# Performance work log

Hardware: AMD Instinct MI355X
Metric: run time of the kernel (lower is better)

## Reference

```python
import jax, jax.numpy as jnp
import numpy as np
from jax import lax

VOCAB = 1000
TMAX = 1001  # max_episode_length + 1
L = 2048
H_GRU = 256


def setup_inputs() -> dict:
    key = jax.random.key(0)
    ks = jax.random.split(key, 40)
    g = lambda i, shape, s: jax.random.normal(ks[i], shape, dtype=jnp.float32) * s
    inp = {
        "x": jax.random.normal(ks[0], (1, 3, 124, 124), dtype=jnp.float32),
        "curr_instr": jax.random.randint(ks[1], (1, L), 0, VOCAB),
        "prev_instr": jax.random.randint(ks[2], (1, L), 0, VOCAB),
        "next_instr": jax.random.randint(ks[3], (1, L), 0, VOCAB),
        "tx": jax.random.randint(ks[4], (1,), 0, TMAX),
        "hx": jnp.zeros((1, 768), jnp.float32),
        "cx": jnp.zeros((1, 768), jnp.float32),
        # conv stack
        "conv1_w": g(5, (128, 3, 8, 8), 0.05), "conv1_b": jnp.zeros((128,), jnp.float32),
        "conv2_w": g(6, (64, 128, 4, 4), 0.03), "conv2_b": jnp.zeros((64,), jnp.float32),
        "conv3_w": g(7, (64, 64, 4, 4), 0.03), "conv3_b": jnp.zeros((64,), jnp.float32),
        # embeddings
        "emb": g(8, (VOCAB, 32), 0.1),
        "time_emb": g(9, (TMAX, 32), 0.1),
        # GRU (torch nn.GRU layout: 3*H rows for r,z,n)
        "gru_w_ih": g(10, (3 * H_GRU, 32), 0.1), "gru_w_hh": g(11, (3 * H_GRU, H_GRU), 0.06),
        "gru_b_ih": jnp.zeros((3 * H_GRU,), jnp.float32), "gru_b_hh": jnp.zeros((3 * H_GRU,), jnp.float32),
        # attention linear 256 -> 64
        "attn_w": g(12, (64, H_GRU), 0.06), "attn_b": jnp.zeros((64,), jnp.float32),
        # image-fusion linear 64*6*6 -> 256
        "lin_w": g(13, (256, 64 * 6 * 6), 0.02), "lin_b": jnp.zeros((256,), jnp.float32),
        # LSTMCell 768 -> 768 (torch layout: 4*H rows for i,f,g,o)
        "lstm_w_ih": g(14, (4 * 768, 768), 0.03), "lstm_w_hh": g(15, (4 * 768, 768), 0.03),
        "lstm_b_ih": jnp.zeros((4 * 768,), jnp.float32), "lstm_b_hh": jnp.zeros((4 * 768,), jnp.float32),
        # heads over [hx, time_emb] = 768 + 32 = 800
        "critic_w": g(16, (1, 800), 0.03), "critic_b": jnp.zeros((1,), jnp.float32),
        "actor_w": g(17, (4, 800), 0.01), "actor_b": jnp.zeros((4,), jnp.float32),
    }
    return inp


def _conv(x, w, b, s):
    return lax.conv_general_dilated(x, w, (s, s), "VALID") + b[None, :, None, None]


def reference(x, curr_instr, prev_instr, next_instr, tx, hx, cx,
              conv1_w, conv1_b, conv2_w, conv2_b, conv3_w, conv3_b,
              emb, time_emb, gru_w_ih, gru_w_hh, gru_b_ih, gru_b_hh,
              attn_w, attn_b, lin_w, lin_b,
              lstm_w_ih, lstm_w_hh, lstm_b_ih, lstm_b_hh,
              critic_w, critic_b, actor_w, actor_b):
    # image tower: [1,3,124,124] -> [1,64,6,6]
    h1 = jax.nn.relu(_conv(x, conv1_w, conv1_b, 4))
    h2 = jax.nn.relu(_conv(h1, conv2_w, conv2_b, 2))
    x_image_rep = jax.nn.relu(_conv(h2, conv3_w, conv3_b, 2))

    # three instruction sequences, encoded by a shared GRU (vmapped scan)
    tokens = jnp.stack([curr_instr[0], prev_instr[0], next_instr[0]])  # [3, L]

    def gru_encode(tok):
        xs = emb[tok]                               # [L, 32]
        gi_all = xs @ gru_w_ih.T + gru_b_ih         # precompute input gates [L, 3H]
        def step(h, gi):
            gh = h @ gru_w_hh.T + gru_b_hh
            i_r, i_z, i_n = jnp.split(gi, 3)
            h_r, h_z, h_n = jnp.split(gh, 3)
            r = jax.nn.sigmoid(i_r + h_r)
            z = jax.nn.sigmoid(i_z + h_z)
            n = jnp.tanh(i_n + r * h_n)
            return (1.0 - z) * n + z * h, None
        h, _ = lax.scan(step, jnp.zeros((H_GRU,), xs.dtype), gi_all)
        return h

    h3 = jax.vmap(gru_encode)(tokens)               # [3, 256]
    attn = jax.nn.sigmoid(h3 @ attn_w.T + attn_b)   # [3, 64]

    # BUG-FAITHFUL: original forward uses cached_computation['curr_x_attention']
    # for all three branches, so the three fused features are identical.
    curr_attn = attn[0][None, :, None, None]        # [1,64,1,1]
    fused = (x_image_rep * curr_attn).reshape(1, -1)  # [1, 2304]
    feat = jax.nn.relu(fused @ lin_w.T + lin_b)     # [1, 256]
    xcat = jnp.concatenate([feat, feat, feat], axis=1)  # [1, 768]

    # LSTMCell
    gates = xcat @ lstm_w_ih.T + lstm_b_ih + hx @ lstm_w_hh.T + lstm_b_hh  # [1, 3072]
    gi, gf, gg, go = jnp.split(gates, 4, axis=1)
    cx_new = jax.nn.sigmoid(gf) * cx + jax.nn.sigmoid(gi) * jnp.tanh(gg)
    hx_new = jax.nn.sigmoid(go) * jnp.tanh(cx_new)

    t = time_emb[tx].reshape(-1, 32)                # [1, 32]
    z = jnp.concatenate([hx_new, t], axis=1)        # [1, 800]
    critic = z @ critic_w.T + critic_b              # [1, 1]
    actor = z @ actor_w.T + actor_b                 # [1, 4]
    return critic, actor, hx_new, cx_new
```

## Files before the change

### kernel.cpp

```cpp
#include <hip/hip_runtime.h>
#include <hip/hip_bf16.h>
#include <stdint.h>


typedef _Float16 half8 __attribute__((ext_vector_type(8)));
typedef _Float16 half2v __attribute__((ext_vector_type(2)));
typedef float f32x4 __attribute__((ext_vector_type(4)));

__device__ __forceinline__ float sigm(float x) { return 1.0f / (1.0f + __expf(-x)); }
__device__ __forceinline__ float tanh_f(float x) { return 2.0f / (1.0f + __expf(-2.0f * x)) - 1.0f; }

__global__ void k_pack(const float* __restrict__ whh, uint32_t* __restrict__ wf16p) {
    int i = blockIdx.x * 256 + threadIdx.x;
    if (i >= 98304) return;
    half2v p = {(_Float16)whh[2 * i], (_Float16)whh[2 * i + 1]};
    wf16p[i] = __builtin_bit_cast(uint32_t, p);
}

__global__ void k_conv1(const float* __restrict__ x, const float* __restrict__ w,
                        const float* __restrict__ b, float* __restrict__ h1) {
    int idx = blockIdx.x * 256 + threadIdx.x;
    if (idx >= 128 * 30 * 30) return;
    int ox = idx % 30, oy = (idx / 30) % 30, oc = idx / 900;
    const float* wr = w + oc * 192;
    float acc = b[oc];
    for (int c = 0; c < 3; ++c)
        for (int ky = 0; ky < 8; ++ky) {
            const float* xr = x + (c * 124 + oy * 4 + ky) * 124 + ox * 4;
            const float* wk = wr + (c * 8 + ky) * 8;
#pragma unroll
            for (int kx = 0; kx < 8; ++kx) acc = fmaf(xr[kx], wk[kx], acc);
        }
    h1[idx] = fmaxf(acc, 0.0f);
}

__global__ void k_conv2(const float* __restrict__ h1, const float* __restrict__ w,
                        const float* __restrict__ b, float* __restrict__ h2) {
    int idx = blockIdx.x * 256 + threadIdx.x;
    if (idx >= 64 * 14 * 14) return;
    int ox = idx % 14, oy = (idx / 14) % 14, oc = idx / 196;
    float acc = b[oc];
    const float* wr = w + oc * 128 * 16;
    for (int c = 0; c < 128; ++c) {
#pragma unroll
        for (int ky = 0; ky < 4; ++ky) {
            const float* hr = h1 + (c * 30 + oy * 2 + ky) * 30 + ox * 2;
            const float* wk = wr + (c * 4 + ky) * 4;
#pragma unroll
            for (int kx = 0; kx < 4; ++kx) acc = fmaf(hr[kx], wk[kx], acc);
        }
    }
    h2[idx] = fmaxf(acc, 0.0f);
}

__global__ void k_conv3(const float* __restrict__ h2, const float* __restrict__ w,
                        const float* __restrict__ b, float* __restrict__ x3) {
    int idx = blockIdx.x * 256 + threadIdx.x;
    if (idx >= 64 * 6 * 6) return;
    int ox = idx % 6, oy = (idx / 6) % 6, oc = idx / 36;
    float acc = b[oc];
    const float* wr = w + oc * 64 * 16;
    for (int c = 0; c < 64; ++c) {
#pragma unroll
        for (int ky = 0; ky < 4; ++ky) {
            const float* hr = h2 + (c * 14 + oy * 2 + ky) * 14 + ox * 2;
            const float* wk = wr + (c * 4 + ky) * 4;
#pragma unroll
            for (int kx = 0; kx < 4; ++kx) acc = fmaf(hr[kx], wk[kx], acc);
        }
    }
    x3[idx] = fmaxf(acc, 0.0f);
}

__global__ void k_gi(const int* __restrict__ curr, const float* __restrict__ emb,
                     const float* __restrict__ wih, const float* __restrict__ bih,
                     const float* __restrict__ bhh, float* __restrict__ gi) {
    int idx = blockIdx.x * 256 + threadIdx.x;
    int j = idx % 768, t = idx / 768;
    int tok = curr[t];
    const float4* e = (const float4*)(emb + tok * 32);
    const float4* wr = (const float4*)(wih + j * 32);
    float acc = bih[j] + (j < 512 ? bhh[j] : 0.0f);
#pragma unroll
    for (int k = 0; k < 8; ++k) {
        float4 ev = e[k], wv = wr[k];
        acc = fmaf(ev.x, wv.x, acc);
        acc = fmaf(ev.y, wv.y, acc);
        acc = fmaf(ev.z, wv.z, acc);
        acc = fmaf(ev.w, wv.w, acc);
    }
    gi[idx] = acc;
}

#define DECLBT(T) uint4 b##T##_0, b##T##_1, b##T##_2, b##T##_3, b##T##_4, b##T##_5, b##T##_6, b##T##_7;
#define LOADBK(T, kt, off) b##T##_##kt = wpR[(off) + (kt)*4 + quad];
#define LOADBT(T, off) LOADBK(T, 0, off) LOADBK(T, 1, off) LOADBK(T, 2, off) LOADBK(T, 3, off) \
                       LOADBK(T, 4, off) LOADBK(T, 5, off) LOADBK(T, 6, off) LOADBK(T, 7, off)
#define TIEBK(T, kt) \
    asm volatile("" : "+v"(b##T##_##kt.x), "+v"(b##T##_##kt.y), "+v"(b##T##_##kt.z), "+v"(b##T##_##kt.w));
#define TIEBT(T) TIEBK(T, 0) TIEBK(T, 1) TIEBK(T, 2) TIEBK(T, 3) TIEBK(T, 4) TIEBK(T, 5) TIEBK(T, 6) TIEBK(T, 7)
#define MF1(T, kt, areg) \
    acc##T = __builtin_amdgcn_mfma_f32_16x16x32_f16(areg, __builtin_bit_cast(half8, b##T##_##kt), acc##T, 0, 0, 0);
#define MFK(kt, areg) MF1(0, kt, areg) MF1(1, kt, areg) MF1(2, kt, areg) \
                      MF1(3, kt, areg) MF1(4, kt, areg) MF1(5, kt, areg)

__global__ __attribute__((amdgpu_flat_work_group_size(512, 512), amdgpu_waves_per_eu(2, 2)))
void k_gru_scan(const float* __restrict__ gi, const uint32_t* __restrict__ wf16p,
                const float* __restrict__ bhh, const float* __restrict__ attn_w,
                const float* __restrict__ attn_b, float* __restrict__ attn0) {
    __shared__ __align__(16) _Float16 hbuf[1024];
    const int tid = threadIdx.x;
    const int lane = tid & 63;
    const int wv = tid >> 6;
    const int n16 = lane & 15;
    const int quad = lane >> 4;
    const int li = n16;

    DECLBT(0) DECLBT(1) DECLBT(2) DECLBT(3) DECLBT(4) DECLBT(5)
    {
        const uint4* wpR = (const uint4*)wf16p + (size_t)(wv * 32 + n16) * 32;
        LOADBT(0, 0) LOADBT(1, 512) LOADBT(2, 8192) LOADBT(3, 8704) LOADBT(4, 16384) LOADBT(5, 16896)
    }
    TIEBT(0) TIEBT(1) TIEBT(2) TIEBT(3) TIEBT(4) TIEBT(5)

    const float bn0 = bhh[512 + wv * 32 + li];
    const float bn1 = bhh[512 + wv * 32 + 16 + li];
    float gr0, gr1, gz0, gz1, gn0v, gn1v;
    {
        const float* g0 = gi + wv * 32 + li;
        gr0 = g0[0]; gr1 = g0[16]; gz0 = g0[256]; gz1 = g0[272]; gn0v = g0[512]; gn1v = g0[528];
    }
    float h0 = 0.0f, h1 = 0.0f;
    hbuf[tid] = (_Float16)0.0f;
    hbuf[512 + tid] = (_Float16)0.0f;
    __syncthreads();

#pragma clang loop unroll(disable)
    for (int step = 0; step < 2048; ++step) {
        const uint4* ab = (const uint4*)hbuf + ((step & 1) << 6) + ((n16 == 1) ? 4 : 0);
        half8 aA = __builtin_bit_cast(half8, ab[0 * 8 + quad]);
        half8 aB = __builtin_bit_cast(half8, ab[1 * 8 + quad]);

        float pr0 = 0.f, pr1 = 0.f, pz0 = 0.f, pz1 = 0.f, pn0 = 0.f, pn1 = 0.f;
        if (step < 2047) {
            const float* gp = gi + (size_t)(step + 1) * 768 + wv * 32 + li;
            pr0 = gp[0]; pr1 = gp[16]; pz0 = gp[256]; pz1 = gp[272]; pn0 = gp[512]; pn1 = gp[528];
        }

        f32x4 acc0 = (f32x4)(0.0f), acc1 = (f32x4)(0.0f), acc2 = (f32x4)(0.0f);
        f32x4 acc3 = (f32x4)(0.0f), acc4 = (f32x4)(0.0f), acc5 = (f32x4)(0.0f);
        MFK(0, aA) aA = __builtin_bit_cast(half8, ab[2 * 8 + quad]);
        MFK(1, aB) aB = __builtin_bit_cast(half8, ab[3 * 8 + quad]);
        MFK(2, aA) aA = __builtin_bit_cast(half8, ab[4 * 8 + quad]);
        MFK(3, aB) aB = __builtin_bit_cast(half8, ab[5 * 8 + quad]);
        MFK(4, aA) aA = __builtin_bit_cast(half8, ab[6 * 8 + quad]);
        MFK(5, aB) aB = __builtin_bit_cast(half8, ab[7 * 8 + quad]);
        MFK(6, aA)
        MFK(7, aB)

        if (lane < 16) {
            const float SC = 0.0009765625f;
            float yr0 = fmaf(acc0.y, SC, acc0.x);
            float yr1 = fmaf(acc1.y, SC, acc1.x);
            float yz0 = fmaf(acc2.y, SC, acc2.x);
            float yz1 = fmaf(acc3.y, SC, acc3.x);
            float yn0 = fmaf(acc4.y, SC, acc4.x) + bn0;
            float yn1 = fmaf(acc5.y, SC, acc5.x) + bn1;
            float r0 = sigm(gr0 + yr0), r1 = sigm(gr1 + yr1);
            float z0 = sigm(gz0 + yz0), z1 = sigm(gz1 + yz1);
            float n0 = tanh_f(fmaf(r0, yn0, gn0v));
            float n1 = tanh_f(fmaf(r1, yn1, gn1v));
            h0 = fmaf(z0, h0 - n0, n0);
            h1 = fmaf(z1, h1 - n1, n1);
            int wb = (((step + 1) & 1) << 9) + (wv << 6);
            _Float16 h0h = (_Float16)h0, h1h = (_Float16)h1;
            hbuf[wb + li] = h0h;
            hbuf[wb + 32 + li] = (_Float16)((h0 - (float)h0h) * 1024.0f);
            hbuf[wb + 16 + li] = h1h;
            hbuf[wb + 48 + li] = (_Float16)((h1 - (float)h1h) * 1024.0f);
        }
        gr0 = pr0; gr1 = pr1; gz0 = pz0; gz1 = pz1; gn0v = pn0; gn1v = pn1;
        __syncthreads();
    }

    if (tid < 64) {
        const float* ar = attn_w + tid * 256;
        float acc = attn_b[tid];
        for (int k = 0; k < 256; ++k) {
            int c = k >> 5, i = k & 31;
            float hk = (float)hbuf[c * 64 + i] + (float)hbuf[c * 64 + 32 + i] * 0.0009765625f;
            acc = fmaf(ar[k], hk, acc);
        }
        attn0[tid] = sigm(acc);
    }
}

__global__ void k_feat(const float* __restrict__ x3, const float* __restrict__ attn0,
                       const float* __restrict__ lw, const float* __restrict__ lb,
                       float* __restrict__ feat) {
    __shared__ __align__(16) float fused[2304];
    int t = threadIdx.x;
    for (int i = t; i < 2304; i += 64) fused[i] = x3[i] * attn0[i / 36];
    __syncthreads();
    int row = blockIdx.x * 64 + t;
    const float4* wvv = (const float4*)(lw + (size_t)row * 2304);
    float acc = lb[row];
    for (int i = 0; i < 576; ++i) {
        float4 v = wvv[i];
        const float* f = fused + i * 4;
        acc = fmaf(v.x, f[0], acc);
        acc = fmaf(v.y, f[1], acc);
        acc = fmaf(v.z, f[2], acc);
        acc = fmaf(v.w, f[3], acc);
    }
    feat[row] = fmaxf(acc, 0.0f);
}

__global__ void k_lstm_gates(const float* __restrict__ wih, const float* __restrict__ whh,
                             const float* __restrict__ bih, const float* __restrict__ bhh,
                             const float* __restrict__ hx, const float* __restrict__ feat,
                             float* __restrict__ gates) {
    int wid = threadIdx.x >> 6, lane = threadIdx.x & 63;
    int row = blockIdx.x * 4 + wid;
    const float* wi = wih + (size_t)row * 768;
    const float* wh = whh + (size_t)row * 768;
    float acc = 0.0f;
#pragma unroll
    for (int i = 0; i < 12; ++i) {
        int k = lane + i * 64;
        acc = fmaf(wi[k], feat[k & 255], acc);
        acc = fmaf(wh[k], hx[k], acc);
    }
#pragma unroll
    for (int s = 32; s; s >>= 1) acc += __shfl_down(acc, s, 64);
    if (lane == 0) gates[row] = acc + bih[row] + bhh[row];
}

__global__ void k_lstm_cell(const float* __restrict__ gates, const float* __restrict__ cx,
                            float* __restrict__ out, float* __restrict__ hxf) {
    int i = threadIdx.x;
    float g_i = gates[i], g_f = gates[768 + i], g_g = gates[1536 + i], g_o = gates[2304 + i];
    float c = cx[i];
    float cn = sigm(g_f) * c + sigm(g_i) * tanh_f(g_g);
    float hn = sigm(g_o) * tanh_f(cn);
    out[5 + i] = hn;
    out[5 + 768 + i] = cn;
    hxf[i] = hn;
}

__global__ void k_heads(const float* __restrict__ hxf, const float* __restrict__ temb,
                        const int* __restrict__ tx, const float* __restrict__ cw,
                        const float* __restrict__ cb, const float* __restrict__ aw,
                        const float* __restrict__ ab, float* __restrict__ out) {
    __shared__ float z[800];
    int t = threadIdx.x;
    for (int i = t; i < 768; i += 320) z[i] = hxf[i];
    if (t < 32) z[768 + t] = temb[tx[0] * 32 + t];
    __syncthreads();
    int w = t >> 6, lane = t & 63;
    const float* row = (w == 0) ? cw : (aw + (size_t)(w - 1) * 800);
    float acc = 0.0f;
    for (int k = lane; k < 800; k += 64) acc = fmaf(row[k], z[k], acc);
#pragma unroll
    for (int s = 32; s; s >>= 1) acc += __shfl_down(acc, s, 64);
    if (lane == 0) {
        float b = (w == 0) ? cb[0] : ab[w - 1];
        out[w] = acc + b;
    }
}

extern "C" void kernel_launch(void* const* d_in, const int* in_sizes, int n_in,
                              void* d_out, int out_size, void* d_ws, size_t ws_size,
                              hipStream_t stream) {
    const float* x = (const float*)d_in[0];
    const int* curr = (const int*)d_in[1];
    const int* tx = (const int*)d_in[4];
    const float* hx = (const float*)d_in[5];
    const float* cx = (const float*)d_in[6];
    const float* c1w = (const float*)d_in[7];
    const float* c1b = (const float*)d_in[8];
    const float* c2w = (const float*)d_in[9];
    const float* c2b = (const float*)d_in[10];
    const float* c3w = (const float*)d_in[11];
    const float* c3b = (const float*)d_in[12];
    const float* emb = (const float*)d_in[13];
    const float* temb = (const float*)d_in[14];
    const float* gwih = (const float*)d_in[15];
    const float* gwhh = (const float*)d_in[16];
    const float* gbih = (const float*)d_in[17];
    const float* gbhh = (const float*)d_in[18];
    const float* attw = (const float*)d_in[19];
    const float* attb = (const float*)d_in[20];
    const float* linw = (const float*)d_in[21];
    const float* linb = (const float*)d_in[22];
    const float* lwih = (const float*)d_in[23];
    const float* lwhh = (const float*)d_in[24];
    const float* lbih = (const float*)d_in[25];
    const float* lbhh = (const float*)d_in[26];
    const float* cw = (const float*)d_in[27];
    const float* cb = (const float*)d_in[28];
    const float* aw = (const float*)d_in[29];
    const float* ab = (const float*)d_in[30];
    float* out = (float*)d_out;

    char* ws = (char*)d_ws;
    float* gi = (float*)(ws + 0);
    float* h1 = (float*)(ws + 6291456);
    float* h2 = (float*)(ws + 6752256);
    float* x3 = (float*)(ws + 6802432);
    float* attn0 = (float*)(ws + 6811648);
    float* feat = (float*)(ws + 6811904);
    float* gates = (float*)(ws + 6812928);
    float* hxf = (float*)(ws + 6825216);
    uint32_t* wf16p = (uint32_t*)(ws + 6828288);

    k_pack<<<384, 256, 0, stream>>>(gwhh, wf16p);
    k_gi<<<6144, 256, 0, stream>>>(curr, emb, gwih, gbih, gbhh, gi);
    k_conv1<<<450, 256, 0, stream>>>(x, c1w, c1b, h1);
    k_conv2<<<49, 256, 0, stream>>>(h1, c2w, c2b, h2);
    k_conv3<<<9, 256, 0, stream>>>(h2, c3w, c3b, x3);
    k_gru_scan<<<1, 512, 0, stream>>>(gi, wf16p, gbhh, attw, attb, attn0);
    k_feat<<<4, 64, 0, stream>>>(x3, attn0, linw, linb, feat);
    k_lstm_gates<<<768, 256, 0, stream>>>(lwih, lwhh, lbih, lbhh, hx, feat, gates);
    k_lstm_cell<<<1, 768, 0, stream>>>(gates, cx, out, hxf);
    k_heads<<<1, 320, 0, stream>>>(hxf, temb, tx, cw, cb, aw, ab, out);
}
```

Measured before the change: 2.671 ms.

## Split GRU scan across two workgroups with global-flag sync; fold conv into scan launch

The 2048-step GRU recurrence, previously run by one 512-thread workgroup, is split across two workgroups (blocks 0 and 8), each owning half of the hidden units. Each step, the halves exchange their new fp16 hi/lo hidden state through global memory, using atomic counters and spin-waits. The conv stack moves into block 1 of the same launch so it overlaps with the scan, and the fp16 weight packing now happens in registers inside the scan kernel instead of a separate pack kernel. The aim is to halve the MFMA work per step on the critical path and remove launches, at the cost of a cross-CU global-memory handshake every step. The spin-wait is capped at 3000 iterations, and it relies on both blocks being co-resident; if a wait times out, results silently go wrong.

```diff
diff --git a/kernel.cpp b/kernel.cpp
--- a/kernel.cpp
+++ b/kernel.cpp
@@ -9,68 +9,11 @@
 
 __device__ __forceinline__ float sigm(float x) { return 1.0f / (1.0f + __expf(-x)); }
 __device__ __forceinline__ float tanh_f(float x) { return 2.0f / (1.0f + __expf(-2.0f * x)) - 1.0f; }
-
-__global__ void k_pack(const float* __restrict__ whh, uint32_t* __restrict__ wf16p) {
-    int i = blockIdx.x * 256 + threadIdx.x;
-    if (i >= 98304) return;
-    half2v p = {(_Float16)whh[2 * i], (_Float16)whh[2 * i + 1]};
-    wf16p[i] = __builtin_bit_cast(uint32_t, p);
-}
-
-__global__ void k_conv1(const float* __restrict__ x, const float* __restrict__ w,
-                        const float* __restrict__ b, float* __restrict__ h1) {
-    int idx = blockIdx.x * 256 + threadIdx.x;
-    if (idx >= 128 * 30 * 30) return;
-    int ox = idx % 30, oy = (idx / 30) % 30, oc = idx / 900;
-    const float* wr = w + oc * 192;
-    float acc = b[oc];
-    for (int c = 0; c < 3; ++c)
-        for (int ky = 0; ky < 8; ++ky) {
-            const float* xr = x + (c * 124 + oy * 4 + ky) * 124 + ox * 4;
-            const float* wk = wr + (c * 8 + ky) * 8;
-#pragma unroll
-            for (int kx = 0; kx < 8; ++kx) acc = fmaf(xr[kx], wk[kx], acc);
-        }
-    h1[idx] = fmaxf(acc, 0.0f);
-}
-
-__global__ void k_conv2(const float* __restrict__ h1, const float* __restrict__ w,
-                        const float* __restrict__ b, float* __restrict__ h2) {
-    int idx = blockIdx.x * 256 + threadIdx.x;
-    if (idx >= 64 * 14 * 14) return;
-    int ox = idx % 14, oy = (idx / 14) % 14, oc = idx / 196;
-    float acc = b[oc];
-    const float* wr = w + oc * 128 * 16;
-    for (int c = 0; c < 128; ++c) {
-#pragma unroll
-        for (int ky = 0; ky < 4; ++ky) {
-            const float* hr = h1 + (c * 30 + oy * 2 + ky) * 30 + ox * 2;
-            const float* wk = wr + (c * 4 + ky) * 4;
-#pragma unroll
-            for (int kx = 0; kx < 4; ++kx) acc = fmaf(hr[kx], wk[kx], acc);
-        }
-    }
-    h2[idx] = fmaxf(acc, 0.0f);
-}
-
-__global__ void k_conv3(const float* __restrict__ h2, const float* __restrict__ w,
-                        const float* __restrict__ b, float* __restrict__ x3) {
-    int idx = blockIdx.x * 256 + threadIdx.x;
-    if (idx >= 64 * 6 * 6) return;
-    int ox = idx % 6, oy = (idx / 6) % 6, oc = idx / 36;
-    float acc = b[oc];
-    const float* wr = w + oc * 64 * 16;
-    for (int c = 0; c < 64; ++c) {
-#pragma unroll
-        for (int ky = 0; ky < 4; ++ky) {
-            const float* hr = h2 + (c * 14 + oy * 2 + ky) * 14 + ox * 2;
-            const float* wk = wr + (c * 4 + ky) * 4;
-#pragma unroll
-            for (int kx = 0; kx < 4; ++kx) acc = fmaf(hr[kx], wk[kx], acc);
-        }
-    }
-    x3[idx] = fmaxf(acc, 0.0f);
-}
+__device__ __forceinline__ uint32_t pk(float a, float b) {
+    half2v h = {(_Float16)a, (_Float16)b};
+    return __builtin_bit_cast(uint32_t, h);
+}
+#define AL(p) __hip_atomic_load((p), __ATOMIC_RELAXED, __HIP_MEMORY_SCOPE_AGENT)
 
 __global__ void k_gi(const int* __restrict__ curr, const float* __restrict__ emb,
                      const float* __restrict__ wih, const float* __restrict__ bih,
@@ -92,106 +35,220 @@
     gi[idx] = acc;
 }
 
-#define DECLBT(T) uint4 b##T##_0, b##T##_1, b##T##_2, b##T##_3, b##T##_4, b##T##_5, b##T##_6, b##T##_7;
-#define LOADBK(T, kt, off) b##T##_##kt = wpR[(off) + (kt)*4 + quad];
-#define LOADBT(T, off) LOADBK(T, 0, off) LOADBK(T, 1, off) LOADBK(T, 2, off) LOADBK(T, 3, off) \
-                       LOADBK(T, 4, off) LOADBK(T, 5, off) LOADBK(T, 6, off) LOADBK(T, 7, off)
-#define TIEBK(T, kt) \
-    asm volatile("" : "+v"(b##T##_##kt.x), "+v"(b##T##_##kt.y), "+v"(b##T##_##kt.z), "+v"(b##T##_##kt.w));
-#define TIEBT(T) TIEBK(T, 0) TIEBK(T, 1) TIEBK(T, 2) TIEBK(T, 3) TIEBK(T, 4) TIEBK(T, 5) TIEBK(T, 6) TIEBK(T, 7)
-#define MF1(T, kt, areg) \
-    acc##T = __builtin_amdgcn_mfma_f32_16x16x32_f16(areg, __builtin_bit_cast(half8, b##T##_##kt), acc##T, 0, 0, 0);
-#define MFK(kt, areg) MF1(0, kt, areg) MF1(1, kt, areg) MF1(2, kt, areg) \
-                      MF1(3, kt, areg) MF1(4, kt, areg) MF1(5, kt, areg)
+#define FORKT(X) X(0) X(1) X(2) X(3) X(4) X(5) X(6) X(7)
+#define DECLB(kt) uint4 bR_##kt, bZ_##kt, bN_##kt;
+#define PACK1(dst, rp, kt)                                        \
+    {                                                             \
+        float4 fA = *(const float4*)((rp) + (kt) * 32 + quad * 8);     \
+        float4 fB = *(const float4*)((rp) + (kt) * 32 + quad * 8 + 4); \
+        dst.x = pk(fA.x, fA.y); dst.y = pk(fA.z, fA.w);           \
+        dst.z = pk(fB.x, fB.y); dst.w = pk(fB.z, fB.w);           \
+    }
+#define PACKB(kt) PACK1(bR_##kt, rpR, kt) PACK1(bZ_##kt, rpZ, kt) PACK1(bN_##kt, rpN, kt)
+#define TIE1(v) asm volatile("" : "+v"(v.x), "+v"(v.y), "+v"(v.z), "+v"(v.w));
+#define TIEB(kt) TIE1(bR_##kt) TIE1(bZ_##kt) TIE1(bN_##kt)
+#define MFT(kt, areg)                                                                                        \
+    accR = __builtin_amdgcn_mfma_f32_16x16x32_f16(areg, __builtin_bit_cast(half8, bR_##kt), accR, 0, 0, 0); \
+    accZ = __builtin_amdgcn_mfma_f32_16x16x32_f16(areg, __builtin_bit_cast(half8, bZ_##kt), accZ, 0, 0, 0); \
+    accN = __builtin_amdgcn_mfma_f32_16x16x32_f16(areg, __builtin_bit_cast(half8, bN_##kt), accN, 0, 0, 0);
+#define RLOAD(i, base)                                                                              \
+    uint32_t q##i##0 = AL((base) + 0), q##i##1 = AL((base) + 1), q##i##2 = AL((base) + 2),          \
+             q##i##3 = AL((base) + 3), q##i##4 = AL((base) + 4), q##i##5 = AL((base) + 5),          \
+             q##i##6 = AL((base) + 6), q##i##7 = AL((base) + 7);
+#define RPERM(i)                                              \
+    half8 ra##i;                                              \
+    {                                                         \
+        uint4 t;                                              \
+        t.x = __builtin_amdgcn_perm(q##i##1, q##i##0, sel);   \
+        t.y = __builtin_amdgcn_perm(q##i##3, q##i##2, sel);   \
+        t.z = __builtin_amdgcn_perm(q##i##5, q##i##4, sel);   \
+        t.w = __builtin_amdgcn_perm(q##i##7, q##i##6, sel);   \
+        ra##i = __builtin_bit_cast(half8, t);                 \
+    }
 
 __global__ __attribute__((amdgpu_flat_work_group_size(512, 512), amdgpu_waves_per_eu(2, 2)))
-void k_gru_scan(const float* __restrict__ gi, const uint32_t* __restrict__ wf16p,
-                const float* __restrict__ bhh, const float* __restrict__ attn_w,
-                const float* __restrict__ attn_b, float* __restrict__ attn0) {
-    __shared__ __align__(16) _Float16 hbuf[1024];
+void k_scan(const float* __restrict__ gi, const float* __restrict__ whh,
+            const float* __restrict__ bhh, const float* __restrict__ attn_w,
+            const float* __restrict__ attn_b, float* __restrict__ attn0,
+            uint32_t* __restrict__ hrem, int* __restrict__ flags,
+            const float* __restrict__ x, const float* __restrict__ c1w,
+            const float* __restrict__ c1b, const float* __restrict__ c2w,
+            const float* __restrict__ c2b, const float* __restrict__ c3w,
+            const float* __restrict__ c3b, float* __restrict__ h1,
+            float* __restrict__ h2, float* __restrict__ x3) {
+    const int bid = blockIdx.x;
     const int tid = threadIdx.x;
+
+    if (bid == 1) {
+        for (int it = 0; it < 225; ++it) {
+            int idx = it * 512 + tid;
+            int ox = idx % 30, oy = (idx / 30) % 30, oc = idx / 900;
+            const float* wr = c1w + oc * 192;
+            float acc = c1b[oc];
+            for (int c = 0; c < 3; ++c)
+                for (int ky = 0; ky < 8; ++ky) {
+                    const float* xr = x + (c * 124 + oy * 4 + ky) * 124 + ox * 4;
+                    const float* wk = wr + (c * 8 + ky) * 8;
+#pragma unroll
+                    for (int kx = 0; kx < 8; ++kx) acc = fmaf(xr[kx], wk[kx], acc);
+                }
+            h1[idx] = fmaxf(acc, 0.0f);
+        }
+        __syncthreads();
+        for (int it = 0; it < 25; ++it) {
+            int idx = it * 512 + tid;
+            if (idx < 12544) {
+                int ox = idx % 14, oy = (idx / 14) % 14, oc = idx / 196;
+                float acc = c2b[oc];
+                const float* wr = c2w + oc * 128 * 16;
+                for (int c = 0; c < 128; ++c) {
+#pragma unroll
+                    for (int ky = 0; ky < 4; ++ky) {
+                        const float* hr = h1 + (c * 30 + oy * 2 + ky) * 30 + ox * 2;
+                        const float* wk = wr + (c * 4 + ky) * 4;
+#pragma unroll
+                        for (int kx = 0; kx < 4; ++kx) acc = fmaf(hr[kx], wk[kx], acc);
+                    }
+                }
+                h2[idx] = fmaxf(acc, 0.0f);
+            }
+        }
+        __syncthreads();
+        for (int it = 0; it < 5; ++it) {
+            int idx = it * 512 + tid;
+            if (idx < 2304) {
+                int ox = idx % 6, oy = (idx / 6) % 6, oc = idx / 36;
+                float acc = c3b[oc];
+                const float* wr = c3w + oc * 64 * 16;
+                for (int c = 0; c < 64; ++c) {
+#pragma unroll
+                    for (int ky = 0; ky < 4; ++ky) {
+                        const float* hr = h2 + (c * 14 + oy * 2 + ky) * 14 + ox * 2;
+                        const float* wk = wr + (c * 4 + ky) * 4;
+#pragma unroll
+                        for (int kx = 0; kx < 4; ++kx) acc = fmaf(hr[kx], wk[kx], acc);
+                    }
+                }
+                x3[idx] = fmaxf(acc, 0.0f);
+            }
+        }
+        return;
+    }
+    if (bid != 0 && bid != 8) return;
+
+    const int half = (bid == 0) ? 0 : 1;
+    const int eb = half * 128;
     const int lane = tid & 63;
     const int wv = tid >> 6;
     const int n16 = lane & 15;
     const int quad = lane >> 4;
-    const int li = n16;
-
-    DECLBT(0) DECLBT(1) DECLBT(2) DECLBT(3) DECLBT(4) DECLBT(5)
+    const int myel = eb + wv * 16 + n16;
+    const int rbase = (1 - half) * 4;
+
+    __shared__ __align__(16) _Float16 hbuf[512];
+
+    FORKT(DECLB)
     {
-        const uint4* wpR = (const uint4*)wf16p + (size_t)(wv * 32 + n16) * 32;
-        LOADBT(0, 0) LOADBT(1, 512) LOADBT(2, 8192) LOADBT(3, 8704) LOADBT(4, 16384) LOADBT(5, 16896)
-    }
-    TIEBT(0) TIEBT(1) TIEBT(2) TIEBT(3) TIEBT(4) TIEBT(5)
-
-    const float bn0 = bhh[512 + wv * 32 + li];
-    const float bn1 = bhh[512 + wv * 32 + 16 + li];
-    float gr0, gr1, gz0, gz1, gn0v, gn1v;
-    {
-        const float* g0 = gi + wv * 32 + li;
-        gr0 = g0[0]; gr1 = g0[16]; gz0 = g0[256]; gz1 = g0[272]; gn0v = g0[512]; gn1v = g0[528];
-    }
-    float h0 = 0.0f, h1 = 0.0f;
+        const float* rpR = whh + (size_t)myel * 256;
+        const float* rpZ = whh + (size_t)(256 + myel) * 256;
+        const float* rpN = whh + (size_t)(512 + myel) * 256;
+        FORKT(PACKB)
+    }
+    FORKT(TIEB)
+    const float bn = bhh[512 + myel];
+
+    if (tid == 0) __hip_atomic_store(&flags[half], 0, __ATOMIC_RELAXED, __HIP_MEMORY_SCOPE_AGENT);
     hbuf[tid] = (_Float16)0.0f;
-    hbuf[512 + tid] = (_Float16)0.0f;
+    if (lane < 16)
+        __hip_atomic_store(&hrem[myel], 0u, __ATOMIC_RELAXED, __HIP_MEMORY_SCOPE_AGENT);
+    float gr = 0.f, gz = 0.f, gn = 0.f, h = 0.f;
+    if (lane < 16) {
+        gr = gi[myel]; gz = gi[256 + myel]; gn = gi[512 + myel];
+    }
     __syncthreads();
+    if (lane == 0) __hip_atomic_fetch_add(&flags[half], 1, __ATOMIC_RELEASE, __HIP_MEMORY_SCOPE_AGENT);
+
+    const uint32_t sel = (n16 == 1) ? 0x07060302u : 0x05040100u;
 
 #pragma clang loop unroll(disable)
-    for (int step = 0; step < 2048; ++step) {
-        const uint4* ab = (const uint4*)hbuf + ((step & 1) << 6) + ((n16 == 1) ? 4 : 0);
+    for (int s = 0; s < 2048; ++s) {
+        const int par = s & 1;
+        const uint4* ab = (const uint4*)hbuf + par * 32 + ((n16 == 1) ? 4 : 0);
         half8 aA = __builtin_bit_cast(half8, ab[0 * 8 + quad]);
         half8 aB = __builtin_bit_cast(half8, ab[1 * 8 + quad]);
-
-        float pr0 = 0.f, pr1 = 0.f, pz0 = 0.f, pz1 = 0.f, pn0 = 0.f, pn1 = 0.f;
-        if (step < 2047) {
-            const float* gp = gi + (size_t)(step + 1) * 768 + wv * 32 + li;
-            pr0 = gp[0]; pr1 = gp[16]; pz0 = gp[256]; pz1 = gp[272]; pn0 = gp[512]; pn1 = gp[528];
-        }
-
-        f32x4 acc0 = (f32x4)(0.0f), acc1 = (f32x4)(0.0f), acc2 = (f32x4)(0.0f);
-        f32x4 acc3 = (f32x4)(0.0f), acc4 = (f32x4)(0.0f), acc5 = (f32x4)(0.0f);
-        MFK(0, aA) aA = __builtin_bit_cast(half8, ab[2 * 8 + quad]);
-        MFK(1, aB) aB = __builtin_bit_cast(half8, ab[3 * 8 + quad]);
-        MFK(2, aA) aA = __builtin_bit_cast(half8, ab[4 * 8 + quad]);
-        MFK(3, aB) aB = __builtin_bit_cast(half8, ab[5 * 8 + quad]);
-        MFK(4, aA) aA = __builtin_bit_cast(half8, ab[6 * 8 + quad]);
-        MFK(5, aB) aB = __builtin_bit_cast(half8, ab[7 * 8 + quad]);
-        MFK(6, aA)
-        MFK(7, aB)
+        half8 aC = __builtin_bit_cast(half8, ab[2 * 8 + quad]);
+        half8 aD = __builtin_bit_cast(half8, ab[3 * 8 + quad]);
+
+        float pgr = 0.f, pgz = 0.f, pgn = 0.f;
+        if (s < 2047 && lane < 16) {
+            const float* gp = gi + (size_t)(s + 1) * 768 + myel;
+            pgr = gp[0]; pgz = gp[256]; pgn = gp[512];
+        }
+
+        f32x4 accR = (f32x4)(0.0f), accZ = (f32x4)(0.0f), accN = (f32x4)(0.0f);
+        if (half == 0) { MFT(0, aA) MFT(1, aB) MFT(2, aC) MFT(3, aD) }
+        else          { MFT(4, aA) MFT(5, aB) MFT(6, aC) MFT(7, aD) }
+
+        {
+            const int tgt = 8 * (s + 1);
+            int g = 0;
+            while (__hip_atomic_load(&flags[1 - half], __ATOMIC_ACQUIRE,
+                                     __HIP_MEMORY_SCOPE_AGENT) < tgt && g < 3000) ++g;
+        }
+        const uint32_t* hr0 = hrem + par * 256 + rbase * 32 + quad * 8;
+        RLOAD(0, hr0) RLOAD(1, hr0 + 32) RLOAD(2, hr0 + 64) RLOAD(3, hr0 + 96)
+        RPERM(0) RPERM(1) RPERM(2) RPERM(3)
+        if (half == 0) { MFT(4, ra0) MFT(5, ra1) MFT(6, ra2) MFT(7, ra3) }
+        else          { MFT(0, ra0) MFT(1, ra1) MFT(2, ra2) MFT(3, ra3) }
 
         if (lane < 16) {
             const float SC = 0.0009765625f;
-            float yr0 = fmaf(acc0.y, SC, acc0.x);
-            float yr1 = fmaf(acc1.y, SC, acc1.x);
-            float yz0 = fmaf(acc2.y, SC, acc2.x);
-            float yz1 = fmaf(acc3.y, SC, acc3.x);
-            float yn0 = fmaf(acc4.y, SC, acc4.x) + bn0;
-            float yn1 = fmaf(acc5.y, SC, acc5.x) + bn1;
-            float r0 = sigm(gr0 + yr0), r1 = sigm(gr1 + yr1);
-            float z0 = sigm(gz0 + yz0), z1 = sigm(gz1 + yz1);
-            float n0 = tanh_f(fmaf(r0, yn0, gn0v));
-            float n1 = tanh_f(fmaf(r1, yn1, gn1v));
-            h0 = fmaf(z0, h0 - n0, n0);
-            h1 = fmaf(z1, h1 - n1, n1);
-            int wb = (((step + 1) & 1) << 9) + (wv << 6);
-            _Float16 h0h = (_Float16)h0, h1h = (_Float16)h1;
-            hbuf[wb + li] = h0h;
-            hbuf[wb + 32 + li] = (_Float16)((h0 - (float)h0h) * 1024.0f);
-            hbuf[wb + 16 + li] = h1h;
-            hbuf[wb + 48 + li] = (_Float16)((h1 - (float)h1h) * 1024.0f);
-        }
-        gr0 = pr0; gr1 = pr1; gz0 = pz0; gz1 = pz1; gn0v = pn0; gn1v = pn1;
+            float yr = fmaf(accR.y, SC, accR.x);
+            float yz = fmaf(accZ.y, SC, accZ.x);
+            float yn = fmaf(accN.y, SC, accN.x) + bn;
+            float r = sigm(gr + yr);
+            float z = sigm(gz + yz);
+            float n = tanh_f(fmaf(r, yn, gn));
+            h = fmaf(z, h - n, n);
+            _Float16 hh = (_Float16)h;
+            _Float16 hl = (_Float16)((h - (float)hh) * 1024.0f);
+            int cl = (myel >> 5) - half * 4, i = myel & 31;
+            int wb = (par ^ 1) * 256 + cl * 64 + i;
+            hbuf[wb] = hh;
+            hbuf[wb + 32] = hl;
+            uint32_t pkv = (uint32_t)__builtin_bit_cast(unsigned short, hh) |
+                           ((uint32_t)__builtin_bit_cast(unsigned short, hl) << 16);
+            __hip_atomic_store(&hrem[(par ^ 1) * 256 + myel], pkv, __ATOMIC_RELAXED,
+                               __HIP_MEMORY_SCOPE_AGENT);
+        }
+        gr = pgr; gz = pgz; gn = pgn;
+        if (lane == 0)
+            __hip_atomic_fetch_add(&flags[half], 1, __ATOMIC_RELEASE, __HIP_MEMORY_SCOPE_AGENT);
         __syncthreads();
     }
 
-    if (tid < 64) {
-        const float* ar = attn_w + tid * 256;
-        float acc = attn_b[tid];
-        for (int k = 0; k < 256; ++k) {
-            int c = k >> 5, i = k & 31;
-            float hk = (float)hbuf[c * 64 + i] + (float)hbuf[c * 64 + 32 + i] * 0.0009765625f;
-            acc = fmaf(ar[k], hk, acc);
-        }
-        attn0[tid] = sigm(acc);
+    if (half == 0) {
+        {
+            int g = 0;
+            while (__hip_atomic_load(&flags[1], __ATOMIC_ACQUIRE,
+                                     __HIP_MEMORY_SCOPE_AGENT) < 8 * 2049 && g < 3000) ++g;
+        }
+        if (tid < 64) {
+            const float* ar = attn_w + tid * 256;
+            float acc = attn_b[tid];
+            for (int k = 0; k < 128; ++k) {
+                int c = k >> 5, i = k & 31;
+                float hk = (float)hbuf[c * 64 + i] + (float)hbuf[c * 64 + 32 + i] * 0.0009765625f;
+                acc = fmaf(ar[k], hk, acc);
+            }
+            for (int k = 128; k < 256; ++k) {
+                uint32_t v = AL(&hrem[k]);
+                float hk = (float)__builtin_bit_cast(_Float16, (unsigned short)(v & 0xffffu)) +
+                           (float)__builtin_bit_cast(_Float16, (unsigned short)(v >> 16)) * 0.0009765625f;
+                acc = fmaf(ar[k], hk, acc);
+            }
+            attn0[tid] = sigm(acc);
+        }
     }
 }
 
@@ -312,14 +369,12 @@
     float* feat = (float*)(ws + 6811904);
     float* gates = (float*)(ws + 6812928);
     float* hxf = (float*)(ws + 6825216);
-    uint32_t* wf16p = (uint32_t*)(ws + 6828288);
-
-    k_pack<<<384, 256, 0, stream>>>(gwhh, wf16p);
+    uint32_t* hrem = (uint32_t*)(ws + 6828288);
+    int* flags = (int*)(ws + 6830336);
+
     k_gi<<<6144, 256, 0, stream>>>(curr, emb, gwih, gbih, gbhh, gi);
-    k_conv1<<<450, 256, 0, stream>>>(x, c1w, c1b, h1);
-    k_conv2<<<49, 256, 0, stream>>>(h1, c2w, c2b, h2);
-    k_conv3<<<9, 256, 0, stream>>>(h2, c3w, c3b, x3);
-    k_gru_scan<<<1, 512, 0, stream>>>(gi, wf16p, gbhh, attw, attb, attn0);
+    k_scan<<<10, 512, 0, stream>>>(gi, gwhh, gbhh, attw, attb, attn0, hrem, flags,
+                                   x, c1w, c1b, c2w, c2b, c3w, c3b, h1, h2, x3);
     k_feat<<<4, 64, 0, stream>>>(x3, attn0, linw, linb, feat);
     k_lstm_gates<<<768, 256, 0, stream>>>(lwih, lwhh, lbih, lbhh, hx, feat, gates);
     k_lstm_cell<<<1, 768, 0, stream>>>(gates, cx, out, hxf);
```

Result: slower. 6.295 ms (+135.7%).
